# Optimization experiments

Hardware: AMD Instinct MI355X
Metric: run time of the kernel (lower is better)

Reference implementation:

```python
import jax, jax.numpy as jnp
import numpy as np

N = 200000   # nodes
R = 4        # relations
E = 1000000  # edges per relation
B = 1024     # graphs in batch


def _graph_conv(h, s, d, ew, W, b):
    """DGL GraphConv, norm='both', optional edge_weight. h:[N,F_in] -> [N,F_out]."""
    n = h.shape[0]
    ones = jnp.ones(s.shape[0], dtype=h.dtype)
    out_deg = jnp.clip(jax.ops.segment_sum(ones, s, num_segments=n), 1.0)
    in_deg = jnp.clip(jax.ops.segment_sum(ones, d, num_segments=n), 1.0)
    hs = h * jax.lax.rsqrt(out_deg)[:, None]          # src-side norm
    m = hs[s]                                         # gather: [E, F_in]
    if ew is not None:
        m = m * ew[:, None]
    agg = jax.ops.segment_sum(m, d, num_segments=n)   # scatter-sum: [N, F_in]
    rst = agg * jax.lax.rsqrt(in_deg)[:, None]        # dst-side norm
    return rst @ W + b


def _hetero_layer(h, src, dst, ew, W, b):
    out = None
    for r in range(R):
        ewr = None if ew is None else ew[r]
        o = _graph_conv(h, src[r], dst[r], ewr, W[r], b[r])
        out = o if out is None else out + o
    return out


def setup_inputs() -> dict:
    key = jax.random.key(0)
    ks = jax.random.split(key, 10)
    feat = jax.random.normal(ks[0], (N, 2), dtype=jnp.float32)
    src = jax.random.randint(ks[1], (R, E), 0, N, dtype=jnp.int32)
    dst = jax.random.randint(ks[2], (R, E), 0, N, dtype=jnp.int32)
    ew = jax.random.uniform(ks[3], (R, E), dtype=jnp.float32)
    graph_ids = jnp.sort(jax.random.randint(ks[4], (N,), 0, B, dtype=jnp.int32))
    W1 = jax.random.normal(ks[5], (R, 2, 16), dtype=jnp.float32) * 0.5
    b1 = jnp.zeros((R, 16), dtype=jnp.float32)
    W2 = jax.random.normal(ks[6], (R, 16, 16), dtype=jnp.float32) * 0.25
    b2 = jnp.zeros((R, 16), dtype=jnp.float32)
    Wc = jax.random.normal(ks[7], (16, 2), dtype=jnp.float32) * 0.25
    bc = jnp.zeros((2,), dtype=jnp.float32)
    return {"feat": feat, "src": src, "dst": dst, "ew": ew,
            "graph_ids": graph_ids, "W1": W1, "b1": b1,
            "W2": W2, "b2": b2, "Wc": Wc, "bc": bc}


def reference(feat, src, dst, ew, graph_ids, W1, b1, W2, b2, Wc, bc):
    # layer 1: per-relation weighted GraphConv, summed over relations
    h = _hetero_layer(feat, src, dst, ew, W1, b1)
    h = jax.nn.relu(h)
    # layer 2: no edge weights (kwargs not forwarded in original code)
    h = _hetero_layer(h, src, dst, None, W2, b2)
    # mean_nodes per graph in the batch
    sums = jax.ops.segment_sum(h, graph_ids, num_segments=B)          # [B,16]
    cnts = jax.ops.segment_sum(jnp.ones((N,), h.dtype), graph_ids, num_segments=B)
    hg = sums / jnp.clip(cnts, 1.0)[:, None]
    return hg @ Wc + bc                                               # [B,2]
```

## Files before the change

### kernel.cpp

```cpp
#include <hip/hip_runtime.h>
#include <hip/hip_fp16.h>

#define NN 200000
#define RR 4
#define EE 1000000
#define BB 1024
#define RN (RR*NN)

#define BSH 7
#define BSZ 128
#define NB 1563
#define RK (RR*NB)
#define EPB 8192
#define BPR ((EE + EPB - 1) / EPB)
#define GSLOTS 32
#define CAPB 1024

#define SRC_OF(u)  (((u) >> 7) & 0x3FFFF)
#define DL_OF(u)   ((int)((u) & 127))
#define DEG_OF(u)  ((u) >> 25)

#define OFF_POOL   0
#define OFF_CNT    (OFF_POOL + BB*16)
#define OFF_GCUR_S (OFF_CNT + BB)
#define OFF_GCUR_D (OFF_GCUR_S + RK)
#define ZERO_UNITS (OFF_GCUR_D + RK)
#define OFF_DEGB   ZERO_UNITS
#define OFF_INVI   (OFF_DEGB + RN/4)
#define OFF_AGG1   (OFF_INVI + RN)
#define OFF_H1H    (OFF_AGG1 + RN*2)
#define OFF_KW_    (OFF_H1H + NN*8)
#define OFF_KW     (OFF_KW_ + (OFF_KW_ & 1))


__global__ __launch_bounds__(512) void k_scat_src(const int* __restrict__ src,
                                                  int* __restrict__ gcur_s,
                                                  unsigned char* __restrict__ srcbin) {
  __shared__ int cnt[NB];
  __shared__ int base[NB];
  __shared__ int lcur[NB];
  int t = threadIdx.x, r = blockIdx.y, c0 = blockIdx.x * EPB;
  for (int i = t; i < NB; i += 512) cnt[i] = 0;
  __syncthreads();
  for (int i = t; i < EPB; i += 512) {
    int e = c0 + i;
    if (e < EE) atomicAdd(&cnt[src[r * EE + e] >> BSH], 1);
  }
  __syncthreads();
  for (int b = t; b < NB; b += 512) {
    int v = cnt[b];
    base[b] = v ? atomicAdd(&gcur_s[r * NB + b], v) : 0;
    lcur[b] = 0;
  }
  __syncthreads();
  for (int i = t; i < EPB; i += 512) {
    int e = c0 + i;
    if (e < EE) {
      int s = src[r * EE + e];
      int b = s >> BSH;
      int off = base[b] + atomicAdd(&lcur[b], 1);
      if (off < CAPB)
        srcbin[(size_t)(r * NB + b) * CAPB + off] = (unsigned char)(s & (BSZ - 1));
    }
  }
}

__global__ __launch_bounds__(128) void k_deg(const unsigned char* __restrict__ srcbin,
                                             const int* __restrict__ gcur_s,
                                             unsigned char* __restrict__ degb) {
  __shared__ int cnt[BSZ];
  int t = threadIdx.x, b = blockIdx.x, r = blockIdx.y;
  cnt[t] = 0;
  __syncthreads();
  int k = r * NB + b;
  size_t st = (size_t)k * CAPB;
  int m = min(gcur_s[k], CAPB);
  for (int e = t; e < m; e += 128) atomicAdd(&cnt[srcbin[st + e]], 1);
  __syncthreads();
  int n = (b << BSH) + t;
  if (n < NN) degb[r * NN + n] = (unsigned char)min(max(cnt[t], 1), 63);
}

__global__ __launch_bounds__(512) void k_scat_dst(const int* __restrict__ src,
                                                  const int* __restrict__ dst,
                                                  const float* __restrict__ ew,
                                                  const unsigned char* __restrict__ degb,
                                                  int* __restrict__ gcur_d,
                                                  long long* __restrict__ kw) {
  __shared__ int cnt[NB];
  __shared__ int base[NB];
  __shared__ int lcur[NB];
  int t = threadIdx.x, r = blockIdx.y, c0 = blockIdx.x * EPB;
  for (int i = t; i < NB; i += 512) cnt[i] = 0;
  __syncthreads();
  for (int i = t; i < EPB; i += 512) {
    int e = c0 + i;
    if (e < EE) atomicAdd(&cnt[dst[r * EE + e] >> BSH], 1);
  }
  __syncthreads();
  for (int b = t; b < NB; b += 512) {
    int v = cnt[b];
    base[b] = v ? atomicAdd(&gcur_d[r * NB + b], v) : 0;
    lcur[b] = 0;
  }
  __syncthreads();
  for (int i = t; i < EPB; i += 512) {
    int e = c0 + i;
    if (e < EE) {
      int idx = r * EE + e;
      int d = dst[idx], s = src[idx];
      int b = d >> BSH;
      int off = base[b] + atomicAdd(&lcur[b], 1);
      if (off < CAPB) {
        unsigned dg = degb[r * NN + s];
        float io = rsqrtf((float)dg);
        unsigned short w1h = __half_as_ushort(__float2half_rn(ew[idx] * io));
        unsigned low = (unsigned)(d & (BSZ - 1)) | ((unsigned)s << 7) | (dg << 25);
        kw[(size_t)(r * NB + b) * CAPB + off] =
            (long long)(((unsigned long long)w1h << 32) | low);
      }
    }
  }
}

__global__ __launch_bounds__(256) void k_l1a(long long* __restrict__ kw,
                                             const int* __restrict__ gcur_d,
                                             const float* __restrict__ feat,
                                             float* __restrict__ invi,
                                             float* __restrict__ agg1) {
  __shared__ long long bufraw[CAPB];
  __shared__ long long bufsort[CAPB];
  __shared__ int cnt[BSZ];
  __shared__ int scn[BSZ];
  __shared__ int cur[BSZ];
  __shared__ float la[BSZ * 3];
  int t = threadIdx.x, b = blockIdx.x, r = blockIdx.y;
  int n0 = b << BSH;
  int k = r * NB + b;
  size_t st = (size_t)k * CAPB;
  int m = min(gcur_d[k], CAPB);
  if (t < BSZ) { cnt[t] = 0; la[t * 3] = 0.f; la[t * 3 + 1] = 0.f; }
  for (int i = t; i < m; i += 256) bufraw[i] = kw[st + i];
  __syncthreads();
  for (int i = t; i < m; i += 256)
    atomicAdd(&cnt[DL_OF((unsigned)bufraw[i])], 1);
  __syncthreads();
  if (t < BSZ) scn[t] = cnt[t];
  __syncthreads();
  for (int off = 1; off < BSZ; off <<= 1) {
    int v = (t < BSZ && t >= off) ? scn[t - off] : 0;
    __syncthreads();
    if (t < BSZ) scn[t] += v;
    __syncthreads();
  }
  if (t < BSZ) {
    cur[t] = scn[t] - cnt[t];
    int n = n0 + t;
    if (n < NN) invi[r * NN + n] = rsqrtf((float)max(cnt[t], 1));
  }
  __syncthreads();
  for (int i = t; i < m; i += 256) {
    long long kv = bufraw[i];
    buf_scatter:
    bufsort[atomicAdd(&cur[DL_OF((unsigned)kv)], 1)] = kv;
  }
  __syncthreads();
  {
    unsigned* up = (unsigned*)kw + 2 * st + CAPB;
    for (int i = t; i < m; i += 256) up[i] = (unsigned)bufsort[i];
  }
  {
    int f = t & 1, grp = t >> 1;
    int seg = (m + BSZ - 1) >> 7;
    int e = grp * seg;
    int e1 = min(e + seg, m);
    float acc = 0.f;
    int dlprev = -1, dlfirst = -1;
    for (; e < e1; e++) {
      long long kv = bufsort[e];
      unsigned low = (unsigned)kv;
      int dl = DL_OF(low);
      int s = SRC_OF(low);
      float w = __half2float(__ushort_as_half((unsigned short)((unsigned long long)kv >> 32)));
      float fv = feat[s * 2 + f];
      if (dl != dlprev) {
        if (dlprev < 0) dlfirst = dl;
        else if (dlprev == dlfirst) atomicAdd(&la[dlprev * 3 + f], acc);
        else la[dlprev * 3 + f] = acc;
        acc = 0.f; dlprev = dl;
      }
      acc += fv * w;
    }
    if (dlprev >= 0) atomicAdd(&la[dlprev * 3 + f], acc);
  }
  __syncthreads();
  if (t < BSZ) {
    int n = n0 + t;
    if (n < NN)
      ((float2*)agg1)[r * NN + n] = make_float2(la[t * 3], la[t * 3 + 1]);
  }
}

__device__ __forceinline__ unsigned pack2h(float a, float b) {
  __half2 h = __floats2half2_rn(a, b);
  return *reinterpret_cast<unsigned*>(&h);
}

__global__ __launch_bounds__(256) void k_l1b(const float* __restrict__ agg1,
                                             const float* __restrict__ invi,
                                             const float* __restrict__ W1,
                                             const float* __restrict__ b1,
                                             __half* __restrict__ h1h) {
  __shared__ float sW[RR * 2 * 16];
  __shared__ float sb[16];
  int t = threadIdx.x, b = blockIdx.x;
  if (t < RR * 2 * 16) sW[t] = W1[t];
  if (t < 16) {
    float s = 0.f;
    for (int r = 0; r < RR; r++) s += b1[r * 16 + t];
    sb[t] = s;
  }
  __syncthreads();
  int n = b * 256 + t;
  if (n >= NN) return;
  float acc[16];
#pragma unroll
  for (int j = 0; j < 16; j++) acc[j] = sb[j];
#pragma unroll
  for (int r = 0; r < RR; r++) {
    float iv = invi[r * NN + n];
    float2 a = ((const float2*)agg1)[r * NN + n];
    float a0 = a.x * iv, a1 = a.y * iv;
#pragma unroll
    for (int j = 0; j < 16; j++)
      acc[j] += a0 * sW[(r * 2 + 0) * 16 + j] + a1 * sW[(r * 2 + 1) * 16 + j];
  }
#pragma unroll
  for (int j = 0; j < 16; j++) acc[j] = fmaxf(acc[j], 0.f);
  uint4 u0, u1;
  u0.x = pack2h(acc[0], acc[1]);  u0.y = pack2h(acc[2], acc[3]);
  u0.z = pack2h(acc[4], acc[5]);  u0.w = pack2h(acc[6], acc[7]);
  u1.x = pack2h(acc[8], acc[9]);  u1.y = pack2h(acc[10], acc[11]);
  u1.z = pack2h(acc[12], acc[13]); u1.w = pack2h(acc[14], acc[15]);
  uint4* o = (uint4*)(h1h + (size_t)n * 16);
  o[0] = u0; o[1] = u1;
}

#define L2P(rec, v)                                                            \
  {                                                                            \
    int dl = DL_OF(rec);                                                       \
    float w = rsqrtf((float)DEG_OF(rec));                                      \
    if (dl != dlprev) {                                                        \
      if (dlprev < 0) dlfirst = dl;                                            \
      else if (dlprev == dlfirst) {                                            \
        atomicAdd(&agg[dlprev * 17 + 2 * f2], a0);                             \
        atomicAdd(&agg[dlprev * 17 + 2 * f2 + 1], a1);                         \
      } else {                                                                 \
        agg[dlprev * 17 + 2 * f2] = a0;                                        \
        agg[dlprev * 17 + 2 * f2 + 1] = a1;                                    \
      }                                                                        \
      a0 = 0.f; a1 = 0.f; dlprev = dl;                                         \
    }                                                                          \
    a0 += (v).x * w; a1 += (v).y * w;                                          \
  }

__global__ __launch_bounds__(256) void k_l2(const long long* __restrict__ kw,
                                            const int* __restrict__ gcur_d,
                                            const __half* __restrict__ h1h,
                                            const float* __restrict__ invi,
                                            const float* __restrict__ W2,
                                            const int* __restrict__ gid,
                                            float* __restrict__ pool,
                                            float* __restrict__ cnt) {
  __shared__ float agg[BSZ * 17];
  __shared__ float sW[16 * 16];
  __shared__ int   sg[BSZ];
  __shared__ float gslot[GSLOTS * 16];
  __shared__ int   cslot[GSLOTS];
  __shared__ int   present[GSLOTS];
  int t = threadIdx.x, b = blockIdx.x, r = blockIdx.y;
  int n0 = b << BSH;
  int k = r * NB + b;
  int m = min(gcur_d[k], CAPB);
  sW[t] = W2[r * 256 + t];
  if (t < GSLOTS) { cslot[t] = 0; present[t] = 0; }
  for (int i = t; i < GSLOTS * 16; i += 256) gslot[i] = 0.f;
  for (int i = t; i < BSZ * 17; i += 256) agg[i] = 0.f;
  __syncthreads();
  const __half2* h2p = (const __half2*)h1h;
  const unsigned* rb = (const unsigned*)kw + 2 * (size_t)k * CAPB + CAPB;
  int f2 = t & 7, g = t >> 3;
  int seg = (m + 31) >> 5;
  int e = g * seg;
  int e1 = min(e + seg, m);
  float a0 = 0.f, a1 = 0.f;
  int dlprev = -1, dlfirst = -1;
  int n4 = (e1 - e) & ~3;
  unsigned c0, c1, c2, c3;
  if (n4) { c0 = rb[e]; c1 = rb[e + 1]; c2 = rb[e + 2]; c3 = rb[e + 3]; }
  for (int i = 0; i < n4; i += 4) {
    unsigned d0 = c0, d1 = c1, d2 = c2, d3 = c3;
    if (i + 4 < n4) {
      c0 = rb[e + 4]; c1 = rb[e + 5]; c2 = rb[e + 6]; c3 = rb[e + 7];
    }
    float2 v0 = __half22float2(h2p[(size_t)SRC_OF(d0) * 8 + f2]);
    float2 v1 = __half22float2(h2p[(size_t)SRC_OF(d1) * 8 + f2]);
    float2 v2 = __half22float2(h2p[(size_t)SRC_OF(d2) * 8 + f2]);
    float2 v3 = __half22float2(h2p[(size_t)SRC_OF(d3) * 8 + f2]);
    L2P(d0, v0);
    L2P(d1, v1);
    L2P(d2, v2);
    L2P(d3, v3);
    e += 4;
  }
  for (; e < e1; e++) {
    unsigned dd = rb[e];
    float2 v = __half22float2(h2p[(size_t)SRC_OF(dd) * 8 + f2]);
    L2P(dd, v);
  }
  if (dlprev >= 0) {
    atomicAdd(&agg[dlprev * 17 + 2 * f2], a0);
    atomicAdd(&agg[dlprev * 17 + 2 * f2 + 1], a1);
  }
  __syncthreads();
  int n = n0 + t;
  int g0 = gid[n0];
  bool valid = (t < BSZ) && (n < NN);
  float acc[16];
#pragma unroll
  for (int j = 0; j < 16; j++) acc[j] = 0.f;
  if (valid) {
    float iv = invi[r * NN + n];
#pragma unroll
    for (int kk = 0; kk < 16; kk++) {
      float a = agg[t * 17 + kk] * iv;
#pragma unroll
      for (int j = 0; j < 16; j++) acc[j] += a * sW[kk * 16 + j];
    }
  }
  __syncthreads();
  if (t < BSZ) {
    sg[t] = valid ? (gid[n] - g0) : -1;
#pragma unroll
    for (int j = 0; j < 16; j++) agg[t * 17 + j] = acc[j];
  }
  __syncthreads();
  {
    int f = t & 15, i0 = t >> 4;
    for (int i = i0; i < BSZ; i += 16) {
      int gsN = sg[i];
      if (gsN < 0) continue;
      float v = agg[i * 17 + f];
      if (gsN < GSLOTS) {
        atomicAdd(&gslot[gsN * 16 + f], v);
        if (f == 0) {
          present[gsN] = 1;
          if (r == 0) atomicAdd(&cslot[gsN], 1);
        }
      } else {
        atomicAdd(&pool[(g0 + gsN) * 16 + f], v);
        if (f == 0 && r == 0) atomicAdd(&cnt[g0 + gsN], 1.0f);
      }
    }
  }
  __syncthreads();
  if (t < GSLOTS * 16) {
    int gsN = t >> 4, f = t & 15;
    if (present[gsN]) atomicAdd(&pool[(g0 + gsN) * 16 + f], gslot[t]);
  }
  if (r == 0 && t < GSLOTS && cslot[t] > 0)
    atomicAdd(&cnt[g0 + t], (float)cslot[t]);
}

__global__ __launch_bounds__(256) void k_final(const float* __restrict__ pool,
                                               const float* __restrict__ cnt,
                                               const float* __restrict__ b2,
                                               const float* __restrict__ Wc,
                                               const float* __restrict__ bc,
                                               float* __restrict__ out) {
  int b = blockIdx.x * 256 + threadIdx.x;
  if (b >= BB) return;
  float c = cnt[b];
  float inv = 1.0f / fmaxf(c, 1.0f);
  float o0 = bc[0], o1 = bc[1];
#pragma unroll
  for (int j = 0; j < 16; j++) {
    float sb = 0.f;
    for (int r = 0; r < RR; r++) sb += b2[r * 16 + j];
    float v = (pool[b * 16 + j] + c * sb) * inv;
    o0 += v * Wc[j * 2 + 0];
    o1 += v * Wc[j * 2 + 1];
  }
  out[b * 2 + 0] = o0;
  out[b * 2 + 1] = o1;
}

extern "C" void kernel_launch(void* const* d_in, const int* in_sizes, int n_in,
                              void* d_out, int out_size, void* d_ws, size_t ws_size,
                              hipStream_t stream) {
  const float* feat = (const float*)d_in[0];
  const int*   src  = (const int*)d_in[1];
  const int*   dst  = (const int*)d_in[2];
  const float* ew   = (const float*)d_in[3];
  const int*   gid  = (const int*)d_in[4];
  const float* W1   = (const float*)d_in[5];
  const float* b1   = (const float*)d_in[6];
  const float* W2   = (const float*)d_in[7];
  const float* b2   = (const float*)d_in[8];
  const float* Wc   = (const float*)d_in[9];
  const float* bc   = (const float*)d_in[10];

  char* ws = (char*)d_ws;
  float* pool   = (float*)(ws + (size_t)OFF_POOL   * 4);
  float* cnt    = (float*)(ws + (size_t)OFF_CNT    * 4);
  int*   gcur_s = (int*)  (ws + (size_t)OFF_GCUR_S * 4);
  int*   gcur_d = (int*)  (ws + (size_t)OFF_GCUR_D * 4);
  unsigned char* degb = (unsigned char*)(ws + (size_t)OFF_DEGB * 4);
  float* invi   = (float*)(ws + (size_t)OFF_INVI   * 4);
  float* agg1   = (float*)(ws + (size_t)OFF_AGG1   * 4);
  __half* h1h   = (__half*)(ws + (size_t)OFF_H1H   * 4);
  long long* kw = (long long*)(ws + (size_t)OFF_KW * 4);

  hipMemsetAsync(d_ws, 0, (size_t)ZERO_UNITS * 4, stream);

  k_scat_src<<<dim3(BPR, RR), 512, 0, stream>>>(src, gcur_s, (unsigned char*)kw);
  k_deg     <<<dim3(NB, RR), 128, 0, stream>>>((const unsigned char*)kw, gcur_s, degb);
  k_scat_dst<<<dim3(BPR, RR), 512, 0, stream>>>(src, dst, ew, degb, gcur_d, kw);
  k_l1a     <<<dim3(NB, RR), 256, 0, stream>>>(kw, gcur_d, feat, invi, agg1);
  k_l1b     <<<(NN + 255) / 256, 256, 0, stream>>>(agg1, invi, W1, b1, h1h);
  k_l2      <<<dim3(NB, RR), 256, 0, stream>>>(kw, gcur_d, h1h, invi, W2, gid, pool, cnt);
  k_final   <<<(BB + 255) / 256, 256, 0, stream>>>(pool, cnt, b2, Wc, bc, (float*)d_out);
}
```

Measured before the change: 377.0 us.

## Store per-node row offsets and gather full 8-half rows per thread in layer 2

Layer-1 aggregation now writes each destination node's exclusive offset into the sorted edge bucket as a 16-bit row pointer. Layer 2 uses these CSR-style offsets so each thread pair owns one destination node and loads 16-byte uint4 rows, one half of the 16-feature row each. This replaces the old equal-split segment scan, with its run-boundary detection and shared-memory atomics, by plain per-node register accumulation. It adds a small extra array write and read, and gives threads uneven work when node degrees differ. The edge-scatter block size is also halved, doubling the number of scatter blocks.

```diff
diff --git a/kernel.cpp b/kernel.cpp
--- a/kernel.cpp
+++ b/kernel.cpp
@@ -11,7 +11,7 @@
 #define BSZ 128
 #define NB 1563
 #define RK (RR*NB)
-#define EPB 8192
+#define EPB 4096
 #define BPR ((EE + EPB - 1) / EPB)
 #define GSLOTS 32
 #define CAPB 1024
@@ -27,7 +27,8 @@
 #define ZERO_UNITS (OFF_GCUR_D + RK)
 #define OFF_DEGB   ZERO_UNITS
 #define OFF_INVI   (OFF_DEGB + RN/4)
-#define OFF_AGG1   (OFF_INVI + RN)
+#define OFF_RW16   (OFF_INVI + RN)
+#define OFF_AGG1   (OFF_RW16 + RN/2)
 #define OFF_H1H    (OFF_AGG1 + RN*2)
 #define OFF_KW_    (OFF_H1H + NN*8)
 #define OFF_KW     (OFF_KW_ + (OFF_KW_ & 1))
@@ -127,6 +128,7 @@
                                              const int* __restrict__ gcur_d,
                                              const float* __restrict__ feat,
                                              float* __restrict__ invi,
+                                             unsigned short* __restrict__ rw16,
                                              float* __restrict__ agg1) {
   __shared__ long long bufraw[CAPB];
   __shared__ long long bufsort[CAPB];
@@ -154,14 +156,17 @@
     __syncthreads();
   }
   if (t < BSZ) {
-    cur[t] = scn[t] - cnt[t];
+    int excl = scn[t] - cnt[t];
+    cur[t] = excl;
     int n = n0 + t;
-    if (n < NN) invi[r * NN + n] = rsqrtf((float)max(cnt[t], 1));
+    if (n < NN) {
+      invi[r * NN + n] = rsqrtf((float)max(cnt[t], 1));
+      rw16[r * NN + n] = (unsigned short)excl;
+    }
   }
   __syncthreads();
   for (int i = t; i < m; i += 256) {
     long long kv = bufraw[i];
-    buf_scatter:
     bufsort[atomicAdd(&cur[DL_OF((unsigned)kv)], 1)] = kv;
   }
   __syncthreads();
@@ -246,26 +251,17 @@
   o[0] = u0; o[1] = u1;
 }
 
-#define L2P(rec, v)                                                            \
-  {                                                                            \
-    int dl = DL_OF(rec);                                                       \
-    float w = rsqrtf((float)DEG_OF(rec));                                      \
-    if (dl != dlprev) {                                                        \
-      if (dlprev < 0) dlfirst = dl;                                            \
-      else if (dlprev == dlfirst) {                                            \
-        atomicAdd(&agg[dlprev * 17 + 2 * f2], a0);                             \
-        atomicAdd(&agg[dlprev * 17 + 2 * f2 + 1], a1);                         \
-      } else {                                                                 \
-        agg[dlprev * 17 + 2 * f2] = a0;                                        \
-        agg[dlprev * 17 + 2 * f2 + 1] = a1;                                    \
-      }                                                                        \
-      a0 = 0.f; a1 = 0.f; dlprev = dl;                                         \
-    }                                                                          \
-    a0 += (v).x * w; a1 += (v).y * w;                                          \
-  }
+__device__ __forceinline__ void acc8(float* acc, uint4 u, float w) {
+  float2 p;
+  p = __half22float2(*(__half2*)&u.x); acc[0] += p.x * w; acc[1] += p.y * w;
+  p = __half22float2(*(__half2*)&u.y); acc[2] += p.x * w; acc[3] += p.y * w;
+  p = __half22float2(*(__half2*)&u.z); acc[4] += p.x * w; acc[5] += p.y * w;
+  p = __half22float2(*(__half2*)&u.w); acc[6] += p.x * w; acc[7] += p.y * w;
+}
 
 __global__ __launch_bounds__(256) void k_l2(const long long* __restrict__ kw,
                                             const int* __restrict__ gcur_d,
+                                            const unsigned short* __restrict__ rw16,
                                             const __half* __restrict__ h1h,
                                             const float* __restrict__ invi,
                                             const float* __restrict__ W2,
@@ -275,6 +271,7 @@
   __shared__ float agg[BSZ * 17];
   __shared__ float sW[16 * 16];
   __shared__ int   sg[BSZ];
+  __shared__ unsigned short srw[BSZ + 1];
   __shared__ float gslot[GSLOTS * 16];
   __shared__ int   cslot[GSLOTS];
   __shared__ int   present[GSLOTS];
@@ -285,64 +282,58 @@
   sW[t] = W2[r * 256 + t];
   if (t < GSLOTS) { cslot[t] = 0; present[t] = 0; }
   for (int i = t; i < GSLOTS * 16; i += 256) gslot[i] = 0.f;
-  for (int i = t; i < BSZ * 17; i += 256) agg[i] = 0.f;
-  __syncthreads();
-  const __half2* h2p = (const __half2*)h1h;
+  if (t < BSZ) {
+    int n = n0 + t;
+    srw[t] = (n < NN) ? rw16[r * NN + n] : (unsigned short)m;
+  }
+  if (t == BSZ) srw[BSZ] = (unsigned short)m;
+  __syncthreads();
+  const uint4* h4p = (const uint4*)h1h;
   const unsigned* rb = (const unsigned*)kw + 2 * (size_t)k * CAPB + CAPB;
-  int f2 = t & 7, g = t >> 3;
-  int seg = (m + 31) >> 5;
-  int e = g * seg;
-  int e1 = min(e + seg, m);
-  float a0 = 0.f, a1 = 0.f;
-  int dlprev = -1, dlfirst = -1;
-  int n4 = (e1 - e) & ~3;
-  unsigned c0, c1, c2, c3;
-  if (n4) { c0 = rb[e]; c1 = rb[e + 1]; c2 = rb[e + 2]; c3 = rb[e + 3]; }
-  for (int i = 0; i < n4; i += 4) {
-    unsigned d0 = c0, d1 = c1, d2 = c2, d3 = c3;
-    if (i + 4 < n4) {
-      c0 = rb[e + 4]; c1 = rb[e + 5]; c2 = rb[e + 6]; c3 = rb[e + 7];
-    }
-    float2 v0 = __half22float2(h2p[(size_t)SRC_OF(d0) * 8 + f2]);
-    float2 v1 = __half22float2(h2p[(size_t)SRC_OF(d1) * 8 + f2]);
-    float2 v2 = __half22float2(h2p[(size_t)SRC_OF(d2) * 8 + f2]);
-    float2 v3 = __half22float2(h2p[(size_t)SRC_OF(d3) * 8 + f2]);
-    L2P(d0, v0);
-    L2P(d1, v1);
-    L2P(d2, v2);
-    L2P(d3, v3);
-    e += 4;
-  }
-  for (; e < e1; e++) {
-    unsigned dd = rb[e];
-    float2 v = __half22float2(h2p[(size_t)SRC_OF(dd) * 8 + f2]);
-    L2P(dd, v);
-  }
-  if (dlprev >= 0) {
-    atomicAdd(&agg[dlprev * 17 + 2 * f2], a0);
-    atomicAdd(&agg[dlprev * 17 + 2 * f2 + 1], a1);
-  }
+  int f8 = t & 1, g = t >> 1;
+  int e = srw[g], en = srw[g + 1];
+  float acc[8];
+#pragma unroll
+  for (int j = 0; j < 8; j++) acc[j] = 0.f;
+  for (; e + 3 < en; e += 4) {
+    unsigned r0 = rb[e], r1 = rb[e + 1], r2 = rb[e + 2], r3 = rb[e + 3];
+    uint4 u0 = h4p[(size_t)SRC_OF(r0) * 2 + f8];
+    uint4 u1 = h4p[(size_t)SRC_OF(r1) * 2 + f8];
+    uint4 u2 = h4p[(size_t)SRC_OF(r2) * 2 + f8];
+    uint4 u3 = h4p[(size_t)SRC_OF(r3) * 2 + f8];
+    acc8(acc, u0, rsqrtf((float)DEG_OF(r0)));
+    acc8(acc, u1, rsqrtf((float)DEG_OF(r1)));
+    acc8(acc, u2, rsqrtf((float)DEG_OF(r2)));
+    acc8(acc, u3, rsqrtf((float)DEG_OF(r3)));
+  }
+  for (; e < en; e++) {
+    unsigned rr = rb[e];
+    uint4 u = h4p[(size_t)SRC_OF(rr) * 2 + f8];
+    acc8(acc, u, rsqrtf((float)DEG_OF(rr)));
+  }
+#pragma unroll
+  for (int j = 0; j < 8; j++) agg[g * 17 + 8 * f8 + j] = acc[j];
   __syncthreads();
   int n = n0 + t;
   int g0 = gid[n0];
   bool valid = (t < BSZ) && (n < NN);
-  float acc[16];
-#pragma unroll
-  for (int j = 0; j < 16; j++) acc[j] = 0.f;
+  float out[16];
+#pragma unroll
+  for (int j = 0; j < 16; j++) out[j] = 0.f;
   if (valid) {
     float iv = invi[r * NN + n];
 #pragma unroll
     for (int kk = 0; kk < 16; kk++) {
       float a = agg[t * 17 + kk] * iv;
 #pragma unroll
-      for (int j = 0; j < 16; j++) acc[j] += a * sW[kk * 16 + j];
+      for (int j = 0; j < 16; j++) out[j] += a * sW[kk * 16 + j];
     }
   }
   __syncthreads();
   if (t < BSZ) {
     sg[t] = valid ? (gid[n] - g0) : -1;
 #pragma unroll
-    for (int j = 0; j < 16; j++) agg[t * 17 + j] = acc[j];
+    for (int j = 0; j < 16; j++) agg[t * 17 + j] = out[j];
   }
   __syncthreads();
   {
@@ -415,8 +406,9 @@
   float* cnt    = (float*)(ws + (size_t)OFF_CNT    * 4);
   int*   gcur_s = (int*)  (ws + (size_t)OFF_GCUR_S * 4);
   int*   gcur_d = (int*)  (ws + (size_t)OFF_GCUR_D * 4);
-  unsigned char* degb = (unsigned char*)(ws + (size_t)OFF_DEGB * 4);
+  unsigned char*  degb = (unsigned char*) (ws + (size_t)OFF_DEGB * 4);
   float* invi   = (float*)(ws + (size_t)OFF_INVI   * 4);
+  unsigned short* rw16 = (unsigned short*)(ws + (size_t)OFF_RW16 * 4);
   float* agg1   = (float*)(ws + (size_t)OFF_AGG1   * 4);
   __half* h1h   = (__half*)(ws + (size_t)OFF_H1H   * 4);
   long long* kw = (long long*)(ws + (size_t)OFF_KW * 4);
@@ -426,8 +418,8 @@
   k_scat_src<<<dim3(BPR, RR), 512, 0, stream>>>(src, gcur_s, (unsigned char*)kw);
   k_deg     <<<dim3(NB, RR), 128, 0, stream>>>((const unsigned char*)kw, gcur_s, degb);
   k_scat_dst<<<dim3(BPR, RR), 512, 0, stream>>>(src, dst, ew, degb, gcur_d, kw);
-  k_l1a     <<<dim3(NB, RR), 256, 0, stream>>>(kw, gcur_d, feat, invi, agg1);
+  k_l1a     <<<dim3(NB, RR), 256, 0, stream>>>(kw, gcur_d, feat, invi, rw16, agg1);
   k_l1b     <<<(NN + 255) / 256, 256, 0, stream>>>(agg1, invi, W1, b1, h1h);
-  k_l2      <<<dim3(NB, RR), 256, 0, stream>>>(kw, gcur_d, h1h, invi, W2, gid, pool, cnt);
+  k_l2      <<<dim3(NB, RR), 256, 0, stream>>>(kw, gcur_d, rw16, h1h, invi, W2, gid, pool, cnt);
   k_final   <<<(BB + 255) / 256, 256, 0, stream>>>(pool, cnt, b2, Wc, bc, (float*)d_out);
 }
```

Measured after the change: 349.4 us. 7.3% less time.
